# Kernel optimization log

Hardware: AMD Instinct MI355X
Metric: run time of the kernel (lower is better)

## Reference

```python
import jax, jax.numpy as jnp
import numpy as np

N = 50000        # n nodes (cells)
C = 1024         # common genes
H = 128          # edge_h_dim
HG = 128         # edge_hidden
E = 1600000      # edges (avg degree 32)
LAYERS = 2       # gnn_layers (unset in original __init__; fixed here)
EPS = 1e-8


def setup_inputs() -> dict:
    key = jax.random.key(0)
    ks = jax.random.split(key, 10)
    x_common = jax.random.normal(ks[0], (N, C), dtype=jnp.float32)
    src = jax.random.randint(ks[1], (E,), 0, N, dtype=jnp.int32)
    dst = jax.random.randint(ks[2], (E,), 0, N, dtype=jnp.int32)
    base_w = jax.random.uniform(ks[3], (E,), dtype=jnp.float32)
    # encoder params: Linear(C,H) -> ReLU -> Linear(H,H) -> ReLU
    W1 = jax.random.normal(ks[4], (C, H), dtype=jnp.float32) * 0.02
    b1 = jnp.zeros((H,), dtype=jnp.float32)
    W2 = jax.random.normal(ks[5], (H, H), dtype=jnp.float32) * 0.1
    b2 = jnp.zeros((H,), dtype=jnp.float32)
    # edge gate params: Linear(2H, HG) -> ReLU -> Linear(HG, 1)
    Wg1 = jax.random.normal(ks[6], (2 * H, HG), dtype=jnp.float32) * 0.1
    bg1 = jnp.zeros((HG,), dtype=jnp.float32)
    Wg2 = jax.random.normal(ks[7], (HG, 1), dtype=jnp.float32) * 0.1
    bg2 = jnp.full((1,), 2.0, dtype=jnp.float32)  # original init: bias=2.0
    # node reliability logits
    rho_raw = jax.random.normal(ks[8], (N,), dtype=jnp.float32) * 0.5
    return dict(x_common=x_common, src=src, dst=dst, base_w=base_w,
                W1=W1, b1=b1, W2=W2, b2=b2,
                Wg1=Wg1, bg1=bg1, Wg2=Wg2, bg2=bg2, rho_raw=rho_raw)


def reference(x_common, src, dst, base_w, W1, b1, W2, b2, Wg1, bg1, Wg2, bg2, rho_raw):
    # enc: [N, C] -> [N, H]
    h = jax.nn.relu(jax.nn.relu(x_common @ W1 + b1) @ W2 + b2)
    rho = jax.nn.sigmoid(rho_raw)                 # [N]
    rr = rho[src] * rho[dst]                      # [E] per-edge reliability factor
    for _ in range(LAYERS):
        h_src = h[src]                            # [E, H] gather
        h_dst = h[dst]                            # [E, H] gather
        z = jnp.concatenate([h_src, h_dst], axis=1)               # [E, 2H]
        gate = jax.nn.sigmoid(jax.nn.relu(z @ Wg1 + bg1) @ Wg2 + bg2)[:, 0]  # [E]
        w = base_w * gate * rr                    # [E]
        m = jax.ops.segment_sum(w[:, None] * h_src, dst, num_segments=N)     # [N, H]
        deg = jax.ops.segment_sum(w, dst, num_segments=N)                    # [N]
        h = m / (deg[:, None] + EPS)
    return h
```

## Files before the change

kernel.cpp:

```cpp
#include <hip/hip_runtime.h>
#include <stdint.h>

#define NN 50000
#define CC 1024
#define HH 128
#define EE 1600000
#define EPSV 1e-8f
#define SCAN_BLKS 196
#define ENC_BLKS 782
#define UV_BLKS 782
#define EDGE_BLKS (EE/256)
#define CONV_BLKS 25000
#define PREP_BLKS 704

typedef __attribute__((ext_vector_type(8))) short bf16x8;
typedef __attribute__((ext_vector_type(4))) float f32x4;
typedef __attribute__((ext_vector_type(2))) float f32x2;

__device__ __forceinline__ unsigned short f32_to_bf16(float f){
  union { float f; uint32_t u; } cv; cv.f = f;
  uint32_t u = cv.u;
  return (unsigned short)((u + 0x7FFFu + ((u >> 16) & 1u)) >> 16);
}
__device__ __forceinline__ float bf16lo_to_f32(uint32_t w){
  union { uint32_t u; float f; } cv; cv.u = w << 16; return cv.f;
}
__device__ __forceinline__ float bf16hi_to_f32(uint32_t w){
  union { uint32_t u; float f; } cv; cv.u = w & 0xFFFF0000u; return cv.f;
}

#define DPP_ADD(x, ctrl) ((x) + __int_as_float(__builtin_amdgcn_update_dpp(0, __float_as_int(x), (ctrl), 0xF, 0xF, true)))

#define GLOAD_LDS16(g, l) __builtin_amdgcn_global_load_lds( \
    (const __attribute__((address_space(1))) uint32_t*)(g), \
    (__attribute__((address_space(3))) uint32_t*)(l), 16, 0, 0)


__global__ __launch_bounds__(256) void k_conv_hist_prep(
    const float* __restrict__ X, unsigned short* __restrict__ Xb,
    const int* __restrict__ src, const int* __restrict__ dst,
    int* __restrict__ counts, int* __restrict__ rank,
    const float* __restrict__ W1, const float* __restrict__ W2,
    const float* __restrict__ Wg1,
    unsigned short* __restrict__ W1T, unsigned short* __restrict__ W2T,
    unsigned short* __restrict__ Wg1T)
{
  const int b = blockIdx.x;
  if(b < CONV_BLKS){
    const size_t i = ((size_t)b*256 + threadIdx.x)*8;
    f32x4 v0 = *(const f32x4*)(X + i);
    f32x4 v1 = *(const f32x4*)(X + i + 4);
    union { bf16x8 v; unsigned short s[8]; } pk;
    #pragma unroll
    for(int j = 0; j < 4; j++){ pk.s[j] = f32_to_bf16(v0[j]); pk.s[4+j] = f32_to_bf16(v1[j]); }
    *(bf16x8*)(Xb + i) = pk.v;
    return;
  }
  if(b < CONV_BLKS + EDGE_BLKS){
    int e = (b - CONV_BLKS)*256 + threadIdx.x;
    if(e < EE) rank[e] = atomicAdd(&counts[dst[e]], 1);
    return;
  }
  int idx = (b - CONV_BLKS - EDGE_BLKS)*256 + threadIdx.x;
  if(idx < 131072){
    int n = idx >> 10, k = idx & 1023;
    W1T[idx] = f32_to_bf16(W1[k*128 + n]);
  } else if(idx < 131072 + 16384){
    int i = idx - 131072;
    int n = i >> 7, k = i & 127;
    W2T[i] = f32_to_bf16(W2[k*128 + n]);
  } else if(idx < 131072 + 16384 + 32768){
    int i = idx - 131072 - 16384;
    int c = i >> 7, k = i & 127;
    int row = (c < 128) ? k : (128 + k);
    int col = (c < 128) ? c : (c - 128);
    Wg1T[i] = f32_to_bf16(Wg1[row*128 + col]);
  }
}


__global__ __launch_bounds__(256) void k_scan1(const int* __restrict__ counts,
    int* __restrict__ lexcl, int* __restrict__ bsum){
  __shared__ int buf[256];
  const int t = threadIdx.x, i = blockIdx.x*256 + t;
  int v = (i < NN) ? counts[i] : 0;
  buf[t] = v;
  __syncthreads();
  for(int off = 1; off < 256; off <<= 1){
    int add = (t >= off) ? buf[t-off] : 0;
    __syncthreads();
    buf[t] += add;
    __syncthreads();
  }
  if(i < NN) lexcl[i] = buf[t] - v;
  if(t == 255) bsum[blockIdx.x] = buf[255];
}

__global__ __launch_bounds__(256) void k_scan2(const int* __restrict__ bsum,
    int* __restrict__ bexcl, int* __restrict__ row_ptr){
  __shared__ int buf[256];
  const int t = threadIdx.x;
  int v = (t < SCAN_BLKS) ? bsum[t] : 0;
  buf[t] = v;
  __syncthreads();
  for(int off = 1; off < 256; off <<= 1){
    int add = (t >= off) ? buf[t-off] : 0;
    __syncthreads();
    buf[t] += add;
    __syncthreads();
  }
  if(t < SCAN_BLKS) bexcl[t] = buf[t] - v;
  if(t == 255) row_ptr[NN] = buf[255];
}

__global__ __launch_bounds__(256) void k_scan3(const int* __restrict__ lexcl,
    const int* __restrict__ bexcl, int* __restrict__ row_ptr){
  const int i = blockIdx.x*256 + threadIdx.x;
  if(i < NN) row_ptr[i] = lexcl[i] + bexcl[blockIdx.x];
}


__global__ __launch_bounds__(256) void k_enc1_fill(
    const unsigned short* __restrict__ Xb, const unsigned short* __restrict__ W1T,
    const float* __restrict__ b1, unsigned short* __restrict__ h1,
    const int* __restrict__ src, const int* __restrict__ dst,
    const float* __restrict__ base_w, const float* __restrict__ rho_raw,
    const int* __restrict__ row_ptr, const int* __restrict__ rank,
    float2* __restrict__ scp)
{
  __shared__ __attribute__((aligned(16))) unsigned short Ab[2][64*32];
  __shared__ __attribute__((aligned(16))) unsigned short Bf[2][128*32];

  if(blockIdx.x >= ENC_BLKS){
    int e = (blockIdx.x - ENC_BLKS)*256 + threadIdx.x;
    if(e < EE){
      int s = src[e], d = dst[e];
      int p = row_ptr[d] + rank[e];
      float rs = 1.f/(1.f + __expf(-rho_raw[s]));
      float rd = 1.f/(1.f + __expf(-rho_raw[d]));
      scp[p] = make_float2(base_w[e]*rs*rd, __int_as_float(s));
    }
    return;
  }

  const int t = threadIdx.x, w = t >> 6, lane = t & 63;
  const int rowL = lane & 15, kq = lane >> 4;
  const int wm = w >> 1, wn = w & 1;
  const int row0 = blockIdx.x * 64;

  const int a_rl  = w*16 + (lane >> 2);
  const int a_cl  = lane & 3;
  const int akeyW = (a_rl ^ (a_rl >> 2)) & 3;
  int agr = row0 + a_rl; if(agr >= NN) agr = NN-1;
  const unsigned short* a_src = Xb + (size_t)agr*1024 + (a_cl ^ akeyW)*8;
  const int b_rl0 = w*32 + (lane >> 2);
  const int b_cl  = lane & 3;
  const int bkey0 = (b_rl0 ^ (b_rl0 >> 2)) & 3;
  const int bkey1 = ((b_rl0+16) ^ ((b_rl0+16) >> 2)) & 3;
  const unsigned short* b_src0 = W1T + (size_t)b_rl0*1024 + (b_cl ^ bkey0)*8;
  const unsigned short* b_src1 = W1T + (size_t)(b_rl0+16)*1024 + (b_cl ^ bkey1)*8;

  #define STAGE(buf, k0)  do{                                              \
    GLOAD_LDS16(a_src  + (k0), &Ab[buf][(w*16)*32]);                       \
    GLOAD_LDS16(b_src0 + (k0), &Bf[buf][(w*32     )*32]);                  \
    GLOAD_LDS16(b_src1 + (k0), &Bf[buf][(w*32 + 16)*32]);                  \
  }while(0)

  f32x4 acc[2][4] = {};
  const int arow0 = wm*32 + rowL;
  const int keyR  = (rowL ^ (rowL >> 2)) & 3;

  auto COMPUTE = [&](const unsigned short* afb, const unsigned short* bfb){
    bf16x8 af[2];
    #pragma unroll
    for(int mf = 0; mf < 2; mf++)
      af[mf] = *(const bf16x8*)&afb[(arow0 + mf*16)*32 + ((kq ^ keyR) << 3)];
    bf16x8 bfr[4];
    #pragma unroll
    for(int nf = 0; nf < 4; nf++){
      const int br = wn*64 + nf*16 + rowL;
      bfr[nf] = *(const bf16x8*)&bfb[br*32 + ((kq ^ keyR) << 3)];
    }
    #pragma unroll
    for(int mf = 0; mf < 2; mf++)
      #pragma unroll
      for(int nf = 0; nf < 4; nf++)
        acc[mf][nf] = __builtin_amdgcn_mfma_f32_16x16x32_bf16(af[mf], bfr[nf], acc[mf][nf], 0, 0, 0);
  };

  #define STEP(cbuf, sbuf, sk)  do{                                        \
    STAGE(sbuf, (sk)*32);                                                  \
    asm volatile("s_waitcnt vmcnt(3)" ::: "memory");                       \
    __builtin_amdgcn_s_barrier();                                          \
    __builtin_amdgcn_sched_barrier(0);                                     \
    COMPUTE(&Ab[cbuf][0], &Bf[cbuf][0]);                                   \
    __builtin_amdgcn_s_barrier();                                          \
  }while(0)

  STAGE(0, 0);
  for(int tt = 0; tt < 30; tt += 2){
    STEP(0, 1, tt + 1);
    STEP(1, 0, tt + 2);
  }
  STEP(0, 1, 31);
  asm volatile("s_waitcnt vmcnt(0)" ::: "memory");
  __builtin_amdgcn_s_barrier();
  __builtin_amdgcn_sched_barrier(0);
  COMPUTE(&Ab[1][0], &Bf[1][0]);
  #undef STEP
  #undef STAGE

  #pragma unroll
  for(int mf = 0; mf < 2; mf++){
    #pragma unroll
    for(int nf = 0; nf < 4; nf++){
      const int col = wn*64 + nf*16 + rowL;
      const float bv = b1[col];
      #pragma unroll
      for(int r = 0; r < 4; r++){
        const int gr = row0 + wm*32 + mf*16 + kq*4 + r;
        if(gr < NN) h1[(size_t)gr*128 + col] = f32_to_bf16(fmaxf(acc[mf][nf][r] + bv, 0.f));
      }
    }
  }
}


__device__ __forceinline__ void uv_phase2(
    const unsigned short* hs, const unsigned short* wgl, int row0, int wave, int lane,
    const float* __restrict__ bg1,
    unsigned short* __restrict__ UH, float* __restrict__ Vf)
{
  const int rowL = lane & 15, kq = lane >> 4;
  const int r = wave*16 + rowL;
  f32x4 acc[16] = {};
  #pragma unroll
  for(int ks = 0; ks < 4; ks++){
    const int kc = ks*4 + kq;
    bf16x8 a = *(const bf16x8*)&hs[r*128 + ((kc ^ (r & 15)) << 3)];
    #pragma unroll
    for(int nt = 0; nt < 16; nt++){
      bf16x8 b = *(const bf16x8*)&wgl[(nt*16 + rowL)*128 + ((kc ^ rowL) << 3)];
      acc[nt] = __builtin_amdgcn_mfma_f32_16x16x32_bf16(a, b, acc[nt], 0, 0, 0);
    }
  }
  #pragma unroll
  for(int nt = 0; nt < 16; nt++){
    const int col = nt*16 + rowL;
    #pragma unroll
    for(int rr = 0; rr < 4; rr++){
      const int gr = row0 + wave*16 + kq*4 + rr;
      if(gr < NN){
        if(col < 128) UH[(size_t)gr*256 + col] = f32_to_bf16(acc[nt][rr]);
        else          Vf[(size_t)gr*128 + col - 128] = acc[nt][rr] + bg1[col - 128];
      }
    }
  }
}


__global__ __launch_bounds__(256) void k_uvA(
    const unsigned short* __restrict__ h1, const unsigned short* __restrict__ W2T,
    const float* __restrict__ b2, const unsigned short* __restrict__ Wg1T,
    const float* __restrict__ bg1, unsigned short* __restrict__ UH,
    float* __restrict__ Vf)
{
  __shared__ __attribute__((aligned(16))) unsigned short hs[64*128];
  __shared__ __attribute__((aligned(16))) unsigned short wgl[256*128];
  const int t = threadIdx.x, wave = t >> 6, lane = t & 63;
  const int rowL = lane & 15, kq = lane >> 4;
  const int row0 = blockIdx.x*64;

  bf16x8 wreg[16];
  #pragma unroll
  for(int i = 0; i < 16; i++)
    wreg[i] = *(const bf16x8*)(Wg1T + (i*256 + t)*8);

  int ar = row0 + wave*16 + rowL; if(ar >= NN) ar = NN-1;
  f32x4 acc[8] = {};
  #pragma unroll
  for(int ks = 0; ks < 4; ks++){
    bf16x8 a = *(const bf16x8*)(h1 + (size_t)ar*128 + ks*32 + kq*8);
    #pragma unroll
    for(int nt = 0; nt < 8; nt++){
      bf16x8 b = *(const bf16x8*)(W2T + (nt*16 + rowL)*128 + ks*32 + kq*8);
      acc[nt] = __builtin_amdgcn_mfma_f32_16x16x32_bf16(a, b, acc[nt], 0, 0, 0);
    }
  }
  #pragma unroll
  for(int nt = 0; nt < 8; nt++){
    const int col = nt*16 + rowL;
    const float bv = b2[col];
    #pragma unroll
    for(int r = 0; r < 4; r++){
      const int rw = wave*16 + kq*4 + r;
      const unsigned short hv = f32_to_bf16(fmaxf(acc[nt][r] + bv, 0.f));
      hs[rw*128 + (((col >> 3) ^ (rw & 15)) << 3) + (col & 7)] = hv;
    }
  }
  #pragma unroll
  for(int i = 0; i < 16; i++){
    const int idx = i*256 + t, row = idx >> 4, c = idx & 15;
    *(bf16x8*)&wgl[row*128 + ((c ^ (row & 15)) << 3)] = wreg[i];
  }
  __syncthreads();
  {
    const int r = t >> 2, gr = row0 + r;
    if(gr < NN){
      #pragma unroll
      for(int j8 = 0; j8 < 4; j8++){
        const int chunk = (t & 3)*4 + j8;
        bf16x8 v = *(const bf16x8*)&hs[r*128 + ((chunk ^ (r & 15)) << 3)];
        *(bf16x8*)&UH[(size_t)gr*256 + 128 + chunk*8] = v;
      }
    }
  }
  uv_phase2(hs, wgl, row0, wave, lane, bg1, UH, Vf);
}


__global__ __launch_bounds__(256) void k_uvB(
    const unsigned short* __restrict__ Wg1T, const float* __restrict__ bg1,
    unsigned short* __restrict__ UH, float* __restrict__ Vf)
{
  __shared__ __attribute__((aligned(16))) unsigned short hs[64*128];
  __shared__ __attribute__((aligned(16))) unsigned short wgl[256*128];
  const int t = threadIdx.x, wave = t >> 6, lane = t & 63;
  const int row0 = blockIdx.x*64;

  bf16x8 wreg[16];
  #pragma unroll
  for(int i = 0; i < 16; i++)
    wreg[i] = *(const bf16x8*)(Wg1T + (i*256 + t)*8);

  {
    const int r = t >> 2, gr0 = row0 + r;
    const int gr = (gr0 < NN) ? gr0 : NN-1;
    const unsigned short* p = UH + (size_t)gr*256 + 128 + (t & 3)*32;
    #pragma unroll
    for(int j8 = 0; j8 < 4; j8++){
      bf16x8 v = *(const bf16x8*)(p + j8*8);
      const int chunk = (t & 3)*4 + j8;
      *(bf16x8*)&hs[r*128 + ((chunk ^ (r & 15)) << 3)] = v;
    }
  }
  #pragma unroll
  for(int i = 0; i < 16; i++){
    const int idx = i*256 + t, row = idx >> 4, c = idx & 15;
    *(bf16x8*)&wgl[row*128 + ((c ^ (row & 15)) << 3)] = wreg[i];
  }
  __syncthreads();
  uv_phase2(hs, wgl, row0, wave, lane, bg1, UH, Vf);
}


__global__ __launch_bounds__(256) void k_gate_agg(
    const unsigned short* __restrict__ UH, const float* __restrict__ Vf,
    const int* __restrict__ row_ptr, const float2* __restrict__ scp,
    const float* __restrict__ Wg2, const float* __restrict__ bg2p,
    float* __restrict__ out_f32, unsigned short* __restrict__ uh_out)
{
  __shared__ float2 ws_s[4][64];
  const int wv = threadIdx.x >> 6, lane = threadIdx.x & 63;
  const int gw = blockIdx.x*4 + wv;
  if(gw >= NN) return;
  const int eq = lane >> 4, li = lane & 15;

  f32x4 va = *(const f32x4*)(Vf + (size_t)gw*128 + li*8);
  f32x4 vb = *(const f32x4*)(Vf + (size_t)gw*128 + li*8 + 4);
  f32x4 wa = *(const f32x4*)(Wg2 + li*8);
  f32x4 wb = *(const f32x4*)(Wg2 + li*8 + 4);
  const float vch[8]  = {va[0],va[1],va[2],va[3],vb[0],vb[1],vb[2],vb[3]};
  const float w2ch[8] = {wa[0],wa[1],wa[2],wa[3],wb[0],wb[1],wb[2],wb[3]};
  const float bg2v = bg2p[0];

  const int beg = row_ptr[gw], end = row_ptr[gw+1];
  float a0 = 0.f, a1 = 0.f, wsum = 0.f;

  for(int base = beg; base < end; base += 64){
    const int nb = min(64, end - base);

    float2 sc_c0, sc_c1; bf16x8 u_c0, u_c1;
    {
      const int i0 = (eq     < nb) ? eq     : 0;
      const int i1 = (4 + eq < nb) ? 4 + eq : 0;
      sc_c0 = scp[base + i0]; sc_c1 = scp[base + i1];
      u_c0 = *(const bf16x8*)&UH[(uint32_t)__float_as_int(sc_c0.y)*256u + li*8];
      u_c1 = *(const bf16x8*)&UH[(uint32_t)__float_as_int(sc_c1.y)*256u + li*8];
    }
    for(int q = 0; q < nb; q += 8){
      float2 sc_n0 = sc_c0, sc_n1 = sc_c1; bf16x8 u_n0 = u_c0, u_n1 = u_c1;
      if(q + 8 < nb){
        const int i0 = (q + 8  + eq < nb) ? q + 8  + eq : 0;
        const int i1 = (q + 12 + eq < nb) ? q + 12 + eq : 0;
        sc_n0 = scp[base + i0]; sc_n1 = scp[base + i1];
        u_n0 = *(const bf16x8*)&UH[(uint32_t)__float_as_int(sc_n0.y)*256u + li*8];
        u_n1 = *(const bf16x8*)&UH[(uint32_t)__float_as_int(sc_n1.y)*256u + li*8];
      }
      {
        union { bf16x8 v; uint32_t u32[4]; } uu; uu.v = u_c0;
        float tacc = 0.f;
        #pragma unroll
        for(int p = 0; p < 4; p++){
          const uint32_t w2b = uu.u32[p];
          tacc += fmaxf(bf16lo_to_f32(w2b) + vch[2*p],   0.f) * w2ch[2*p];
          tacc += fmaxf(bf16hi_to_f32(w2b) + vch[2*p+1], 0.f) * w2ch[2*p+1];
        }
        tacc = DPP_ADD(tacc, 0xB1);
        tacc = DPP_ADD(tacc, 0x4E);
        tacc = DPP_ADD(tacc, 0x141);
        tacc = DPP_ADD(tacc, 0x140);
        const float g = 1.f/(1.f + __expf(-(tacc + bg2v)));
        const int idx = q + eq;
        if(li == 0 && idx < nb) ws_s[wv][idx] = make_float2(sc_c0.x*g, sc_c0.y);
      }
      {
        union { bf16x8 v; uint32_t u32[4]; } uu; uu.v = u_c1;
        float tacc = 0.f;
        #pragma unroll
        for(int p = 0; p < 4; p++){
          const uint32_t w2b = uu.u32[p];
          tacc += fmaxf(bf16lo_to_f32(w2b) + vch[2*p],   0.f) * w2ch[2*p];
          tacc += fmaxf(bf16hi_to_f32(w2b) + vch[2*p+1], 0.f) * w2ch[2*p+1];
        }
        tacc = DPP_ADD(tacc, 0xB1);
        tacc = DPP_ADD(tacc, 0x4E);
        tacc = DPP_ADD(tacc, 0x141);
        tacc = DPP_ADD(tacc, 0x140);
        const float g = 1.f/(1.f + __expf(-(tacc + bg2v)));
        const int idx = q + 4 + eq;
        if(li == 0 && idx < nb) ws_s[wv][idx] = make_float2(sc_c1.x*g, sc_c1.y);
      }
      sc_c0 = sc_n0; sc_c1 = sc_n1; u_c0 = u_n0; u_c1 = u_n1;
    }

    #pragma unroll 8
    for(int j = 0; j < nb; j++){
      const float2 p = ws_s[wv][j];
      const float w  = p.x;
      const uint32_t s = (uint32_t)__float_as_int(p.y);
      const uint32_t hw = *(const uint32_t*)&UH[s*256u + 128u + lane*2];
      a0 += w*bf16lo_to_f32(hw);
      a1 += w*bf16hi_to_f32(hw);
      wsum += w;
    }
  }
  const float inv = 1.f/(wsum + EPSV);
  const float r0 = a0*inv, r1 = a1*inv;
  if(uh_out){
    const uint32_t packed = (uint32_t)f32_to_bf16(r0) | ((uint32_t)f32_to_bf16(r1) << 16);
    *(uint32_t*)&uh_out[(size_t)gw*256 + 128 + lane*2] = packed;
  } else {
    const size_t o = (size_t)gw*128 + lane*2;
    *(f32x2*)&out_f32[o] = (f32x2){r0, r1};
  }
}


extern "C" void kernel_launch(void* const* d_in, const int* in_sizes, int n_in,
                              void* d_out, int out_size, void* d_ws, size_t ws_size,
                              hipStream_t stream) {
  (void)in_sizes; (void)n_in; (void)out_size; (void)ws_size;
  const float* X      = (const float*)d_in[0];
  const int*   src    = (const int*)d_in[1];
  const int*   dst    = (const int*)d_in[2];
  const float* base_w = (const float*)d_in[3];
  const float* W1     = (const float*)d_in[4];
  const float* b1     = (const float*)d_in[5];
  const float* W2     = (const float*)d_in[6];
  const float* b2     = (const float*)d_in[7];
  const float* Wg1    = (const float*)d_in[8];
  const float* bg1    = (const float*)d_in[9];
  const float* Wg2    = (const float*)d_in[10];
  const float* bg2    = (const float*)d_in[11];
  const float* rho    = (const float*)d_in[12];

  char* ws = (char*)d_ws;
  size_t off = 0;
  auto alloc = [&](size_t bytes)->char*{ char* p = ws + off; off += (bytes + 255) & ~(size_t)255; return p; };
  unsigned short* W1T      = (unsigned short*)alloc((size_t)1024*128*2);
  unsigned short* W2T      = (unsigned short*)alloc((size_t)128*128*2);
  unsigned short* Wg1T     = (unsigned short*)alloc((size_t)256*128*2);
  int*            rank     = (int*)alloc((size_t)EE*4);
  float2*         scp      = (float2*)alloc((size_t)EE*8);
  int*            row_ptr  = (int*)alloc((size_t)(NN+1)*4);
  int*            counts   = (int*)alloc((size_t)NN*4);
  int*            lexcl    = (int*)alloc((size_t)NN*4);
  int*            bsum     = (int*)alloc((size_t)256*4);
  int*            bexcl    = (int*)alloc((size_t)256*4);
  unsigned short* h1       = (unsigned short*)alloc((size_t)NN*128*2);
  unsigned short* UH_A     = (unsigned short*)alloc((size_t)NN*256*2);
  unsigned short* UH_B     = (unsigned short*)alloc((size_t)NN*256*2);
  float*          Vf       = (float*)alloc((size_t)NN*128*4);
  unsigned short* Xb       = (unsigned short*)alloc((size_t)NN*CC*2);

  hipMemsetAsync(counts, 0, (size_t)NN*4, stream);
  k_conv_hist_prep<<<CONV_BLKS + EDGE_BLKS + PREP_BLKS, 256, 0, stream>>>(
      X, Xb, src, dst, counts, rank, W1, W2, Wg1, W1T, W2T, Wg1T);

  k_scan1<<<SCAN_BLKS, 256, 0, stream>>>(counts, lexcl, bsum);
  k_scan2<<<1, 256, 0, stream>>>(bsum, bexcl, row_ptr);
  k_scan3<<<SCAN_BLKS, 256, 0, stream>>>(lexcl, bexcl, row_ptr);

  k_enc1_fill<<<ENC_BLKS + EDGE_BLKS, 256, 0, stream>>>(
      Xb, W1T, b1, h1, src, dst, base_w, rho, row_ptr, rank, scp);

  k_uvA<<<UV_BLKS, 256, 0, stream>>>(h1, W2T, b2, Wg1T, bg1, UH_A, Vf);

  k_gate_agg<<<12500, 256, 0, stream>>>(UH_A, Vf, row_ptr, scp, Wg2, bg2, nullptr, UH_B);
  k_uvB<<<UV_BLKS, 256, 0, stream>>>(Wg1T, bg1, UH_B, Vf);
  k_gate_agg<<<12500, 256, 0, stream>>>(UH_B, Vf, row_ptr, scp, Wg2, bg2, (float*)d_out, nullptr);
}
```

Baseline: 493.2 us.

## Reorder prep blocks, fuse scan passes, keep gate weights in registers

Three independent changes. The prep kernel now runs histogram and weight-transpose blocks ahead of the bf16 conversion of X, so the atomics start earlier. The single-block scan2 is removed: each scan3 block computes its own prefix of the block sums, which saves one launch. The UV kernels no longer stage the 64 KB Wg1 tile in LDS; each wave loads its 64-column slice of Wg1T into registers and loops over four row tiles. This cuts LDS use and should raise occupancy, at the cost of more registers and redundant global/L2 weight reads per block.

```diff
diff --git a/kernel.cpp b/kernel.cpp
--- a/kernel.cpp
+++ b/kernel.cpp
@@ -46,36 +46,36 @@
     unsigned short* __restrict__ Wg1T)
 {
   const int b = blockIdx.x;
-  if(b < CONV_BLKS){
-    const size_t i = ((size_t)b*256 + threadIdx.x)*8;
-    f32x4 v0 = *(const f32x4*)(X + i);
-    f32x4 v1 = *(const f32x4*)(X + i + 4);
-    union { bf16x8 v; unsigned short s[8]; } pk;
-    #pragma unroll
-    for(int j = 0; j < 4; j++){ pk.s[j] = f32_to_bf16(v0[j]); pk.s[4+j] = f32_to_bf16(v1[j]); }
-    *(bf16x8*)(Xb + i) = pk.v;
-    return;
-  }
-  if(b < CONV_BLKS + EDGE_BLKS){
-    int e = (b - CONV_BLKS)*256 + threadIdx.x;
+  if(b < EDGE_BLKS){
+    int e = b*256 + threadIdx.x;
     if(e < EE) rank[e] = atomicAdd(&counts[dst[e]], 1);
     return;
   }
-  int idx = (b - CONV_BLKS - EDGE_BLKS)*256 + threadIdx.x;
-  if(idx < 131072){
-    int n = idx >> 10, k = idx & 1023;
-    W1T[idx] = f32_to_bf16(W1[k*128 + n]);
-  } else if(idx < 131072 + 16384){
-    int i = idx - 131072;
-    int n = i >> 7, k = i & 127;
-    W2T[i] = f32_to_bf16(W2[k*128 + n]);
-  } else if(idx < 131072 + 16384 + 32768){
-    int i = idx - 131072 - 16384;
-    int c = i >> 7, k = i & 127;
-    int row = (c < 128) ? k : (128 + k);
-    int col = (c < 128) ? c : (c - 128);
-    Wg1T[i] = f32_to_bf16(Wg1[row*128 + col]);
-  }
+  if(b < EDGE_BLKS + PREP_BLKS){
+    int idx = (b - EDGE_BLKS)*256 + threadIdx.x;
+    if(idx < 131072){
+      int n = idx >> 10, k = idx & 1023;
+      W1T[idx] = f32_to_bf16(W1[k*128 + n]);
+    } else if(idx < 131072 + 16384){
+      int i = idx - 131072;
+      int n = i >> 7, k = i & 127;
+      W2T[i] = f32_to_bf16(W2[k*128 + n]);
+    } else if(idx < 131072 + 16384 + 32768){
+      int i = idx - 131072 - 16384;
+      int c = i >> 7, k = i & 127;
+      int row = (c < 128) ? k : (128 + k);
+      int col = (c < 128) ? c : (c - 128);
+      Wg1T[i] = f32_to_bf16(Wg1[row*128 + col]);
+    }
+    return;
+  }
+  const size_t i = (((size_t)(b - EDGE_BLKS - PREP_BLKS))*256 + threadIdx.x)*8;
+  f32x4 v0 = *(const f32x4*)(X + i);
+  f32x4 v1 = *(const f32x4*)(X + i + 4);
+  union { bf16x8 v; unsigned short s[8]; } pk;
+  #pragma unroll
+  for(int j = 0; j < 4; j++){ pk.s[j] = f32_to_bf16(v0[j]); pk.s[4+j] = f32_to_bf16(v1[j]); }
+  *(bf16x8*)(Xb + i) = pk.v;
 }
 
 
@@ -96,27 +96,22 @@
   if(t == 255) bsum[blockIdx.x] = buf[255];
 }
 
-__global__ __launch_bounds__(256) void k_scan2(const int* __restrict__ bsum,
-    int* __restrict__ bexcl, int* __restrict__ row_ptr){
-  __shared__ int buf[256];
-  const int t = threadIdx.x;
-  int v = (t < SCAN_BLKS) ? bsum[t] : 0;
-  buf[t] = v;
+__global__ __launch_bounds__(256) void k_scan3(const int* __restrict__ lexcl,
+    const int* __restrict__ bsum, int* __restrict__ row_ptr){
+  __shared__ int red[256];
+  const int t = threadIdx.x, b = blockIdx.x;
+  red[t] = (t < b) ? bsum[t] : 0;
   __syncthreads();
   for(int off = 1; off < 256; off <<= 1){
-    int add = (t >= off) ? buf[t-off] : 0;
+    int add = (t >= off) ? red[t-off] : 0;
     __syncthreads();
-    buf[t] += add;
+    red[t] += add;
     __syncthreads();
   }
-  if(t < SCAN_BLKS) bexcl[t] = buf[t] - v;
-  if(t == 255) row_ptr[NN] = buf[255];
-}
-
-__global__ __launch_bounds__(256) void k_scan3(const int* __restrict__ lexcl,
-    const int* __restrict__ bexcl, int* __restrict__ row_ptr){
-  const int i = blockIdx.x*256 + threadIdx.x;
-  if(i < NN) row_ptr[i] = lexcl[i] + bexcl[blockIdx.x];
+  const int bexcl = red[255];
+  const int i = b*256 + t;
+  if(i < NN) row_ptr[i] = lexcl[i] + bexcl;
+  if(i == 0) row_ptr[NN] = EE;
 }
 
 
@@ -227,32 +222,40 @@
 
 
 __device__ __forceinline__ void uv_phase2(
-    const unsigned short* hs, const unsigned short* wgl, int row0, int wave, int lane,
-    const float* __restrict__ bg1,
+    const unsigned short* hs, int row0, int w, int lane,
+    const unsigned short* __restrict__ Wg1T, const float* __restrict__ bg1,
     unsigned short* __restrict__ UH, float* __restrict__ Vf)
 {
   const int rowL = lane & 15, kq = lane >> 4;
-  const int r = wave*16 + rowL;
-  f32x4 acc[16] = {};
-  #pragma unroll
-  for(int ks = 0; ks < 4; ks++){
-    const int kc = ks*4 + kq;
-    bf16x8 a = *(const bf16x8*)&hs[r*128 + ((kc ^ (r & 15)) << 3)];
-    #pragma unroll
-    for(int nt = 0; nt < 16; nt++){
-      bf16x8 b = *(const bf16x8*)&wgl[(nt*16 + rowL)*128 + ((kc ^ rowL) << 3)];
-      acc[nt] = __builtin_amdgcn_mfma_f32_16x16x32_bf16(a, b, acc[nt], 0, 0, 0);
-    }
-  }
-  #pragma unroll
-  for(int nt = 0; nt < 16; nt++){
-    const int col = nt*16 + rowL;
-    #pragma unroll
-    for(int rr = 0; rr < 4; rr++){
-      const int gr = row0 + wave*16 + kq*4 + rr;
-      if(gr < NN){
-        if(col < 128) UH[(size_t)gr*256 + col] = f32_to_bf16(acc[nt][rr]);
-        else          Vf[(size_t)gr*128 + col - 128] = acc[nt][rr] + bg1[col - 128];
+  bf16x8 breg[4][4];
+  #pragma unroll
+  for(int nt = 0; nt < 4; nt++)
+    #pragma unroll
+    for(int ks = 0; ks < 4; ks++)
+      breg[nt][ks] = *(const bf16x8*)(Wg1T + (size_t)(w*64 + nt*16 + rowL)*128 + ks*32 + kq*8);
+
+  #pragma unroll
+  for(int mt = 0; mt < 4; mt++){
+    const int r = mt*16 + rowL;
+    f32x4 acc[4] = {};
+    #pragma unroll
+    for(int ks = 0; ks < 4; ks++){
+      const int kc = ks*4 + kq;
+      bf16x8 a = *(const bf16x8*)&hs[r*128 + ((kc ^ rowL) << 3)];
+      #pragma unroll
+      for(int nt = 0; nt < 4; nt++)
+        acc[nt] = __builtin_amdgcn_mfma_f32_16x16x32_bf16(a, breg[nt][ks], acc[nt], 0, 0, 0);
+    }
+    #pragma unroll
+    for(int nt = 0; nt < 4; nt++){
+      const int col = w*64 + nt*16 + rowL;
+      #pragma unroll
+      for(int rr = 0; rr < 4; rr++){
+        const int gr = row0 + mt*16 + kq*4 + rr;
+        if(gr < NN){
+          if(col < 128) UH[(size_t)gr*256 + col] = f32_to_bf16(acc[nt][rr]);
+          else          Vf[(size_t)gr*128 + col - 128] = acc[nt][rr] + bg1[col - 128];
+        }
       }
     }
   }
@@ -266,15 +269,9 @@
     float* __restrict__ Vf)
 {
   __shared__ __attribute__((aligned(16))) unsigned short hs[64*128];
-  __shared__ __attribute__((aligned(16))) unsigned short wgl[256*128];
   const int t = threadIdx.x, wave = t >> 6, lane = t & 63;
   const int rowL = lane & 15, kq = lane >> 4;
   const int row0 = blockIdx.x*64;
-
-  bf16x8 wreg[16];
-  #pragma unroll
-  for(int i = 0; i < 16; i++)
-    wreg[i] = *(const bf16x8*)(Wg1T + (i*256 + t)*8);
 
   int ar = row0 + wave*16 + rowL; if(ar >= NN) ar = NN-1;
   f32x4 acc[8] = {};
@@ -297,11 +294,6 @@
       const unsigned short hv = f32_to_bf16(fmaxf(acc[nt][r] + bv, 0.f));
       hs[rw*128 + (((col >> 3) ^ (rw & 15)) << 3) + (col & 7)] = hv;
     }
-  }
-  #pragma unroll
-  for(int i = 0; i < 16; i++){
-    const int idx = i*256 + t, row = idx >> 4, c = idx & 15;
-    *(bf16x8*)&wgl[row*128 + ((c ^ (row & 15)) << 3)] = wreg[i];
   }
   __syncthreads();
   {
@@ -315,7 +307,7 @@
       }
     }
   }
-  uv_phase2(hs, wgl, row0, wave, lane, bg1, UH, Vf);
+  uv_phase2(hs, row0, wave, lane, Wg1T, bg1, UH, Vf);
 }
 
 
@@ -324,14 +316,8 @@
     unsigned short* __restrict__ UH, float* __restrict__ Vf)
 {
   __shared__ __attribute__((aligned(16))) unsigned short hs[64*128];
-  __shared__ __attribute__((aligned(16))) unsigned short wgl[256*128];
   const int t = threadIdx.x, wave = t >> 6, lane = t & 63;
   const int row0 = blockIdx.x*64;
-
-  bf16x8 wreg[16];
-  #pragma unroll
-  for(int i = 0; i < 16; i++)
-    wreg[i] = *(const bf16x8*)(Wg1T + (i*256 + t)*8);
 
   {
     const int r = t >> 2, gr0 = row0 + r;
@@ -344,13 +330,8 @@
       *(bf16x8*)&hs[r*128 + ((chunk ^ (r & 15)) << 3)] = v;
     }
   }
-  #pragma unroll
-  for(int i = 0; i < 16; i++){
-    const int idx = i*256 + t, row = idx >> 4, c = idx & 15;
-    *(bf16x8*)&wgl[row*128 + ((c ^ (row & 15)) << 3)] = wreg[i];
-  }
   __syncthreads();
-  uv_phase2(hs, wgl, row0, wave, lane, bg1, UH, Vf);
+  uv_phase2(hs, row0, wave, lane, Wg1T, bg1, UH, Vf);
 }
 
 
@@ -487,7 +468,6 @@
   int*            counts   = (int*)alloc((size_t)NN*4);
   int*            lexcl    = (int*)alloc((size_t)NN*4);
   int*            bsum     = (int*)alloc((size_t)256*4);
-  int*            bexcl    = (int*)alloc((size_t)256*4);
   unsigned short* h1       = (unsigned short*)alloc((size_t)NN*128*2);
   unsigned short* UH_A     = (unsigned short*)alloc((size_t)NN*256*2);
   unsigned short* UH_B     = (unsigned short*)alloc((size_t)NN*256*2);
@@ -495,12 +475,11 @@
   unsigned short* Xb       = (unsigned short*)alloc((size_t)NN*CC*2);
 
   hipMemsetAsync(counts, 0, (size_t)NN*4, stream);
-  k_conv_hist_prep<<<CONV_BLKS + EDGE_BLKS + PREP_BLKS, 256, 0, stream>>>(
+  k_conv_hist_prep<<<EDGE_BLKS + PREP_BLKS + CONV_BLKS, 256, 0, stream>>>(
       X, Xb, src, dst, counts, rank, W1, W2, Wg1, W1T, W2T, Wg1T);
 
   k_scan1<<<SCAN_BLKS, 256, 0, stream>>>(counts, lexcl, bsum);
-  k_scan2<<<1, 256, 0, stream>>>(bsum, bexcl, row_ptr);
-  k_scan3<<<SCAN_BLKS, 256, 0, stream>>>(lexcl, bexcl, row_ptr);
+  k_scan3<<<SCAN_BLKS, 256, 0, stream>>>(lexcl, bsum, row_ptr);
 
   k_enc1_fill<<<ENC_BLKS + EDGE_BLKS, 256, 0, stream>>>(
       Xb, W1T, b1, h1, src, dst, base_w, rho, row_ptr, rank, scp);
```

Result: no change. 493.8 us (+0.1%).
